# Kernel tuning notes

Measured on AMD Instinct MI355X. Metric: run time of the kernel, lower is better.

The kernel has to match this reference:

```python
import jax, jax.numpy as jnp
import numpy as np

B, V, J, H, W = 32, 2, 17, 128, 128
TEMP = 0.05   # SoftArgmax2D softmax_temp
EPS = 1e-12


def _soft_argmax(hm):
    # hm: (B*V, J, H, W) -> homogeneous coords (B*V, 3, J), per-joint max value
    bv, j, h, w = hm.shape
    p = jax.nn.softmax(hm.reshape(bv, j, h * w) / TEMP, axis=-1).reshape(bv, j, h, w)
    xs = jnp.arange(w, dtype=hm.dtype)
    ys = jnp.arange(h, dtype=hm.dtype)
    x = jnp.einsum('bjhw,w->bj', p, xs)
    y = jnp.einsum('bjhw,h->bj', p, ys)
    coords = jnp.stack([x, y, jnp.ones_like(x)], axis=1)  # (bv, 3, j)
    maxv = hm.max(axis=(-2, -1))
    return coords, maxv


def _skew(t):
    # t: (..., 3) -> skew-symmetric (..., 3, 3), matches -t_mat^T + t_mat in source
    tx, ty, tz = t[..., 0], t[..., 1], t[..., 2]
    z = jnp.zeros_like(tx)
    return jnp.stack([jnp.stack([z, -tz, ty], -1),
                      jnp.stack([tz, z, -tx], -1),
                      jnp.stack([-ty, tx, z], -1)], -2)


def _forward(origin_hms, AP_K, AP_T, LAT_K, LAT_T):
    K = jnp.stack([AP_K, LAT_K], axis=1)              # (B,V,3,3)
    T = jnp.stack([AP_T, LAT_T], axis=1)              # (B,V,4,4)
    R = T[:, :, :3, :3]
    t_std = T[:, :, :3, 3]                            # (B,V,3) standard_cam_T

    # fundamental matrices for all ordered pairs: cam1 = view j, cam2 = view i
    r = jnp.einsum('bimk,bjnk->bijmn', R, R)          # R_i @ R_j^T
    t = t_std[:, :, None, :] - jnp.einsum('bijmn,bjn->bijm', r, t_std)
    M = jnp.einsum('bijmn,bijnk->bijmk', _skew(t), r)
    invK = jnp.linalg.inv(K)
    # F = invK_i^T @ [t]x @ r @ invK_j
    F = jnp.einsum('bipm,bijpq,bjql->bijml', invK, M, invK)  # (B,V,V,3,3)

    coords, maxv = _soft_argmax(origin_hms)           # (B*V,3,J), (B*V,J)
    inv_aff = jnp.diag(jnp.asarray([4.0, 4.0, 1.0], dtype=origin_hms.dtype))  # inverse of 0.25 scale
    img = jnp.einsum('mn,bvnj->bvmj', inv_aff, coords.reshape(B, V, 3, J))
    confi = maxv.reshape(B, V, J)

    # epipolar distances, fully vectorized over (b, i, j) pairs
    l = jnp.einsum('bijmn,bjnk->bijmk', F, img)       # epipolar lines in view i from joints of view j
    cv = img[:, :, None]                              # (B,V,1,3,J)
    num = jnp.sum(cv * l, axis=3) ** 2                # (B,V,V,J)
    lp = jnp.einsum('bijnm,bink->bijmk', F, img)      # F^T @ cv_joints
    div = l[..., 0, :] ** 2 + l[..., 1, :] ** 2 + lp[..., 0, :] ** 2 + lp[..., 1, :] ** 2
    dist_full = jnp.sqrt(num / (div + EPS))           # (B,V,V,J)

    others = np.asarray([[j for j in range(V) if j != i] for i in range(V)])  # (V,V-1)
    ii = np.repeat(np.arange(V)[:, None], V - 1, axis=1)
    distances = dist_full[:, ii, others]              # (B,V,V-1,J)

    # stand-in for ViewWeightNet: confidence minus mean epipolar error, softmax over views
    score = confi - distances.mean(axis=2)            # (B,V,J)
    vw = jax.nn.softmax(score, axis=1)                # (B,V,J)

    mv = jnp.where(maxv > 0.01, maxv, 1e6).reshape(B * V, J, 1, 1)
    hms_norm = origin_hms / mv
    hm4 = hms_norm.reshape(B, V, J, H, W)

    # cat order: self heatmap first, then other views (matches get_warp_weight / cat_hm layout)
    order = np.asarray([[i] + [j for j in range(V) if j != i] for i in range(V)])  # (V,V)
    cat_hm = hm4[:, order]                            # (B,V,V,J,H,W); identity-warp stand-in for CamFusionModule
    ww = vw[:, order]                                 # (B,V,V,J) warp weights
    fused_hm = jnp.sum(ww[..., None, None] * cat_hm, axis=2).reshape(B * V, J, H, W)

    coords2, _ = _soft_argmax(fused_hm)
    img2 = jnp.einsum('mn,bvnj->bvmj', inv_aff, coords2.reshape(B, V, 3, J))
    return img2[:, :, :2, :], fused_hm


def setup_inputs() -> dict:
    key = jax.random.key(0)
    k1, k2, k3, k4, k5 = jax.random.split(key, 5)
    hms = jax.random.uniform(k1, (B * V, J, H, W), dtype=jnp.float32)

    def make_K(k):
        f = 1000.0 + jax.random.normal(k, (B,)) * 10.0
        Km = jnp.zeros((B, 3, 3), dtype=jnp.float32)
        Km = Km.at[:, 0, 0].set(f).at[:, 1, 1].set(f)
        Km = Km.at[:, 0, 2].set(256.0).at[:, 1, 2].set(256.0).at[:, 2, 2].set(1.0)
        return Km

    def make_T(k):
        A = jax.random.normal(k, (B, 3, 3))
        Q, _ = jnp.linalg.qr(A)
        Q = Q * jnp.linalg.det(Q)[:, None, None]  # force det = +1 (proper rotation)
        t = jax.random.normal(jax.random.fold_in(k, 1), (B, 3, 1)) * 0.1 + jnp.asarray([0.0, 0.0, 5.0]).reshape(3, 1)
        bottom = jnp.tile(jnp.asarray([[[0.0, 0.0, 0.0, 1.0]]]), (B, 1, 1))
        return jnp.concatenate([jnp.concatenate([Q, t], axis=2), bottom], axis=1).astype(jnp.float32)

    return {"origin_hms": hms, "AP_K": make_K(k2), "AP_T": make_T(k3),
            "LAT_K": make_K(k4), "LAT_T": make_T(k5)}


def reference(origin_hms, AP_K, AP_T, LAT_K, LAT_T):
    return _forward(origin_hms, AP_K, AP_T, LAT_K, LAT_T)
```

## Files before the change

### kernel.cpp

```cpp
#include <hip/hip_runtime.h>
#include <math.h>

#define NB 32
#define NV 2
#define NJ 17
#define NH 128
#define NW 128
#define MAPN (NH * NW)
#define MAPN4 (MAPN / 4)
#define NMAPS (NB * NV * NJ)
#define NBJ (NB * NJ)
#define OUT0N (NB * NV * 2 * NJ)
#define INV_TEMP 20.0f
#define EPS_D 1e-12f

typedef float vfloat4 __attribute__((ext_vector_type(4)));

__device__ __forceinline__ float waveMax(float v) {
#pragma unroll
    for (int off = 32; off > 0; off >>= 1)
        v = fmaxf(v, __shfl_xor(v, off, 64));
    return v;
}
__device__ __forceinline__ float waveSum(float v) {
#pragma unroll
    for (int off = 32; off > 0; off >>= 1)
        v += __shfl_xor(v, off, 64);
    return v;
}

__device__ __forceinline__ void inv3(const float K[3][3], float o[3][3]) {
    const float a = K[0][0], b = K[0][1], c = K[0][2];
    const float d = K[1][0], e = K[1][1], f = K[1][2];
    const float g = K[2][0], h = K[2][1], i = K[2][2];
    const float A =  (e * i - f * h);
    const float Bv = -(d * i - f * g);
    const float C =  (d * h - e * g);
    const float det = a * A + b * Bv + c * C;
    const float id = 1.0f / det;
    o[0][0] = A * id;  o[0][1] = -(b * i - c * h) * id;  o[0][2] = (b * f - c * e) * id;
    o[1][0] = Bv * id; o[1][1] = (a * i - c * g) * id;   o[1][2] = -(a * f - c * d) * id;
    o[2][0] = C * id;  o[2][1] = -(a * h - b * g) * id;  o[2][2] = (a * e - b * d) * id;
}

__global__ __launch_bounds__(512, 4) void k_all(const float* __restrict__ hms,
                                                const float* __restrict__ APK,
                                                const float* __restrict__ APT,
                                                const float* __restrict__ LATK,
                                                const float* __restrict__ LATT,
                                                float* __restrict__ out) {
    const int blk = blockIdx.x;
    const int b = blk / NJ, j = blk % NJ;
    const int tid = threadIdx.x;
    const int wid = tid >> 6, lane = tid & 63;

    const size_t m0 = ((size_t)(b * 2 + 0) * NJ + j) * MAPN4;
    const size_t m1 = ((size_t)(b * 2 + 1) * NJ + j) * MAPN4;
    const float4* A  = (const float4*)hms + m0;
    const float4* Bm = (const float4*)hms + m1;

    float4 va[8], vb[8];
#pragma unroll
    for (int u = 0; u < 8; ++u) {
        va[u] = A[tid + u * 512];
        vb[u] = Bm[tid + u * 512];
    }

    float mx0 = -1e30f, mx1 = -1e30f;
    float s0 = 0.f, sx0 = 0.f, sy0 = 0.f;
    float s1 = 0.f, sx1 = 0.f, sy1 = 0.f;
#pragma unroll
    for (int u = 0; u < 8; ++u) {
        const int e0 = (tid + u * 512) * 4;
        const float hh = (float)(e0 >> 7);
        const float ww = (float)(e0 & 127);
        {
            const float4 v = va[u];
            mx0 = fmaxf(mx0, fmaxf(fmaxf(v.x, v.y), fmaxf(v.z, v.w)));
            const float ea = __expf((v.x - 1.0f) * INV_TEMP);
            const float eb = __expf((v.y - 1.0f) * INV_TEMP);
            const float ec = __expf((v.z - 1.0f) * INV_TEMP);
            const float ed = __expf((v.w - 1.0f) * INV_TEMP);
            const float se = (ea + eb) + (ec + ed);
            s0 += se; sy0 += se * hh;
            sx0 += ea * ww + eb * (ww + 1.f) + ec * (ww + 2.f) + ed * (ww + 3.f);
        }
        {
            const float4 v = vb[u];
            mx1 = fmaxf(mx1, fmaxf(fmaxf(v.x, v.y), fmaxf(v.z, v.w)));
            const float ea = __expf((v.x - 1.0f) * INV_TEMP);
            const float eb = __expf((v.y - 1.0f) * INV_TEMP);
            const float ec = __expf((v.z - 1.0f) * INV_TEMP);
            const float ed = __expf((v.w - 1.0f) * INV_TEMP);
            const float se = (ea + eb) + (ec + ed);
            s1 += se; sy1 += se * hh;
            sx1 += ea * ww + eb * (ww + 1.f) + ec * (ww + 2.f) + ed * (ww + 3.f);
        }
    }

    __shared__ float red[8][8];
    __shared__ float wsh[2];
    mx0 = waveMax(mx0); mx1 = waveMax(mx1);
    s0 = waveSum(s0); sx0 = waveSum(sx0); sy0 = waveSum(sy0);
    s1 = waveSum(s1); sx1 = waveSum(sx1); sy1 = waveSum(sy1);
    if (lane == 0) {
        red[0][wid] = mx0; red[1][wid] = s0; red[2][wid] = sx0; red[3][wid] = sy0;
        red[4][wid] = mx1; red[5][wid] = s1; red[6][wid] = sx1; red[7][wid] = sy1;
    }
    __syncthreads();

    if (tid == 0) {
        float M0 = red[0][0], S0 = red[1][0], SX0 = red[2][0], SY0 = red[3][0];
        float M1 = red[4][0], S1 = red[5][0], SX1 = red[6][0], SY1 = red[7][0];
#pragma unroll
        for (int w = 1; w < 8; ++w) {
            M0 = fmaxf(M0, red[0][w]); S0 += red[1][w]; SX0 += red[2][w]; SY0 += red[3][w];
            M1 = fmaxf(M1, red[4][w]); S1 += red[5][w]; SX1 += red[6][w]; SY1 += red[7][w];
        }
        const float conf[2] = {M0, M1};
        float img[2][3];
        img[0][0] = 4.0f * (SX0 / S0); img[0][1] = 4.0f * (SY0 / S0); img[0][2] = 1.0f;
        img[1][0] = 4.0f * (SX1 / S1); img[1][1] = 4.0f * (SY1 / S1); img[1][2] = 1.0f;

        float Km[2][3][3], R[2][3][3], tr[2][3], iK[2][3][3];
        for (int r = 0; r < 3; ++r)
            for (int c = 0; c < 3; ++c) {
                Km[0][r][c] = APK[b * 9 + r * 3 + c];
                Km[1][r][c] = LATK[b * 9 + r * 3 + c];
                R[0][r][c] = APT[b * 16 + r * 4 + c];
                R[1][r][c] = LATT[b * 16 + r * 4 + c];
            }
        for (int r = 0; r < 3; ++r) {
            tr[0][r] = APT[b * 16 + r * 4 + 3];
            tr[1][r] = LATT[b * 16 + r * 4 + 3];
        }
        inv3(Km[0], iK[0]);
        inv3(Km[1], iK[1]);

        float F[2][3][3];
        for (int i = 0; i < 2; ++i) {
            const int jj = 1 - i;
            float r[3][3];
            for (int m = 0; m < 3; ++m)
                for (int n = 0; n < 3; ++n)
                    r[m][n] = R[i][m][0] * R[jj][n][0] + R[i][m][1] * R[jj][n][1] + R[i][m][2] * R[jj][n][2];
            float tv[3];
            for (int m = 0; m < 3; ++m)
                tv[m] = tr[i][m] - (r[m][0] * tr[jj][0] + r[m][1] * tr[jj][1] + r[m][2] * tr[jj][2]);
            const float S[3][3] = {{0.f, -tv[2], tv[1]}, {tv[2], 0.f, -tv[0]}, {-tv[1], tv[0], 0.f}};
            float M[3][3];
            for (int m = 0; m < 3; ++m)
                for (int n = 0; n < 3; ++n)
                    M[m][n] = S[m][0] * r[0][n] + S[m][1] * r[1][n] + S[m][2] * r[2][n];
            float tmp[3][3];
            for (int p = 0; p < 3; ++p)
                for (int l = 0; l < 3; ++l)
                    tmp[p][l] = M[p][0] * iK[jj][0][l] + M[p][1] * iK[jj][1][l] + M[p][2] * iK[jj][2][l];
            for (int m = 0; m < 3; ++m)
                for (int l = 0; l < 3; ++l)
                    F[i][m][l] = iK[i][0][m] * tmp[0][l] + iK[i][1][m] * tmp[1][l] + iK[i][2][m] * tmp[2][l];
        }

        float score[2];
        for (int i = 0; i < 2; ++i) {
            const int jj = 1 - i;
            const float l0 = F[i][0][0] * img[jj][0] + F[i][0][1] * img[jj][1] + F[i][0][2] * img[jj][2];
            const float l1 = F[i][1][0] * img[jj][0] + F[i][1][1] * img[jj][1] + F[i][1][2] * img[jj][2];
            const float l2 = F[i][2][0] * img[jj][0] + F[i][2][1] * img[jj][1] + F[i][2][2] * img[jj][2];
            const float sdot = img[i][0] * l0 + img[i][1] * l1 + img[i][2] * l2;
            const float num = sdot * sdot;
            const float lp0 = F[i][0][0] * img[i][0] + F[i][1][0] * img[i][1] + F[i][2][0] * img[i][2];
            const float lp1 = F[i][0][1] * img[i][0] + F[i][1][1] * img[i][1] + F[i][2][1] * img[i][2];
            const float dv = l0 * l0 + l1 * l1 + lp0 * lp0 + lp1 * lp1;
            score[i] = conf[i] - sqrtf(num / (dv + EPS_D));
        }

        const float mS = fmaxf(score[0], score[1]);
        const float e0 = __expf(score[0] - mS), e1 = __expf(score[1] - mS);
        const float inv = 1.0f / (e0 + e1);
        const float mv0 = conf[0] > 0.01f ? conf[0] : 1e6f;
        const float mv1 = conf[1] > 0.01f ? conf[1] : 1e6f;
        wsh[0] = (e0 * inv) / mv0;
        wsh[1] = (e1 * inv) / mv1;
    }
    __syncthreads();
    const float w0 = wsh[0];
    const float w1 = wsh[1];

    float* outhm = out + OUT0N;
    vfloat4* O0 = reinterpret_cast<vfloat4*>(outhm) + m0;
    vfloat4* O1 = reinterpret_cast<vfloat4*>(outhm) + m1;

    float s = 0.f, sx = 0.f, sy = 0.f;
#pragma unroll
    for (int u = 0; u < 8; ++u) {
        const int i4 = tid + u * 512;
        const float4 a = va[u];
        const float4 c = vb[u];
        vfloat4 f;
        f.x = w0 * a.x + w1 * c.x;
        f.y = w0 * a.y + w1 * c.y;
        f.z = w0 * a.z + w1 * c.z;
        f.w = w0 * a.w + w1 * c.w;
        __builtin_nontemporal_store(f, &O0[i4]);
        __builtin_nontemporal_store(f, &O1[i4]);
        const int e0 = i4 * 4;
        const float hh = (float)(e0 >> 7);
        const float ww = (float)(e0 & 127);
        const float ea = __expf((f.x - 1.0f) * INV_TEMP);
        const float eb = __expf((f.y - 1.0f) * INV_TEMP);
        const float ec = __expf((f.z - 1.0f) * INV_TEMP);
        const float ed = __expf((f.w - 1.0f) * INV_TEMP);
        const float se = (ea + eb) + (ec + ed);
        s += se; sy += se * hh;
        sx += ea * ww + eb * (ww + 1.f) + ec * (ww + 2.f) + ed * (ww + 3.f);
    }

    s = waveSum(s); sx = waveSum(sx); sy = waveSum(sy);
    if (lane == 0) { red[0][wid] = s; red[1][wid] = sx; red[2][wid] = sy; }
    __syncthreads();
    if (tid == 0) {
        float S = red[0][0], SX = red[1][0], SY = red[2][0];
#pragma unroll
        for (int w = 1; w < 8; ++w) { S += red[0][w]; SX += red[1][w]; SY += red[2][w]; }
        const float x4 = 4.0f * (SX / S);
        const float y4 = 4.0f * (SY / S);
        out[((b * 2 + 0) * 2 + 0) * NJ + j] = x4;
        out[((b * 2 + 0) * 2 + 1) * NJ + j] = y4;
        out[((b * 2 + 1) * 2 + 0) * NJ + j] = x4;
        out[((b * 2 + 1) * 2 + 1) * NJ + j] = y4;
    }
}

extern "C" void kernel_launch(void* const* d_in, const int* in_sizes, int n_in,
                              void* d_out, int out_size, void* d_ws, size_t ws_size,
                              hipStream_t stream) {
    const float* hms  = (const float*)d_in[0];
    const float* APK  = (const float*)d_in[1];
    const float* APT  = (const float*)d_in[2];
    const float* LATK = (const float*)d_in[3];
    const float* LATT = (const float*)d_in[4];
    float* out = (float*)d_out;

    k_all<<<NBJ, 512, 0, stream>>>(hms, APK, APT, LATK, LATT, out);
}
```

Measured before the change: 141.7 us.

## Compute F redundantly per thread, drop vb register cache, reload view-1 map

Every thread now computes the fundamental matrices and the fusion weights redundantly. This removes the single-thread serial section and one barrier round trip. The view-1 map is no longer kept in registers and is reloaded from global memory (likely an L2 hit) in the fuse pass, which cuts register pressure. The launch bound's minimum-blocks hint drops from 4 to 2 to give the compiler more register room. In exchange, each thread does more redundant scalar math and the kernel issues a second read of one input map.

```diff
diff --git a/kernel.cpp b/kernel.cpp
--- a/kernel.cpp
+++ b/kernel.cpp
@@ -43,7 +43,7 @@
     o[2][0] = C * id;  o[2][1] = -(a * h - b * g) * id;  o[2][2] = (a * e - b * d) * id;
 }
 
-__global__ __launch_bounds__(512, 4) void k_all(const float* __restrict__ hms,
+__global__ __launch_bounds__(512, 2) void k_one(const float* __restrict__ hms,
                                                 const float* __restrict__ APK,
                                                 const float* __restrict__ APT,
                                                 const float* __restrict__ LATK,
@@ -54,74 +54,8 @@
     const int tid = threadIdx.x;
     const int wid = tid >> 6, lane = tid & 63;
 
-    const size_t m0 = ((size_t)(b * 2 + 0) * NJ + j) * MAPN4;
-    const size_t m1 = ((size_t)(b * 2 + 1) * NJ + j) * MAPN4;
-    const float4* A  = (const float4*)hms + m0;
-    const float4* Bm = (const float4*)hms + m1;
-
-    float4 va[8], vb[8];
-#pragma unroll
-    for (int u = 0; u < 8; ++u) {
-        va[u] = A[tid + u * 512];
-        vb[u] = Bm[tid + u * 512];
-    }
-
-    float mx0 = -1e30f, mx1 = -1e30f;
-    float s0 = 0.f, sx0 = 0.f, sy0 = 0.f;
-    float s1 = 0.f, sx1 = 0.f, sy1 = 0.f;
-#pragma unroll
-    for (int u = 0; u < 8; ++u) {
-        const int e0 = (tid + u * 512) * 4;
-        const float hh = (float)(e0 >> 7);
-        const float ww = (float)(e0 & 127);
-        {
-            const float4 v = va[u];
-            mx0 = fmaxf(mx0, fmaxf(fmaxf(v.x, v.y), fmaxf(v.z, v.w)));
-            const float ea = __expf((v.x - 1.0f) * INV_TEMP);
-            const float eb = __expf((v.y - 1.0f) * INV_TEMP);
-            const float ec = __expf((v.z - 1.0f) * INV_TEMP);
-            const float ed = __expf((v.w - 1.0f) * INV_TEMP);
-            const float se = (ea + eb) + (ec + ed);
-            s0 += se; sy0 += se * hh;
-            sx0 += ea * ww + eb * (ww + 1.f) + ec * (ww + 2.f) + ed * (ww + 3.f);
-        }
-        {
-            const float4 v = vb[u];
-            mx1 = fmaxf(mx1, fmaxf(fmaxf(v.x, v.y), fmaxf(v.z, v.w)));
-            const float ea = __expf((v.x - 1.0f) * INV_TEMP);
-            const float eb = __expf((v.y - 1.0f) * INV_TEMP);
-            const float ec = __expf((v.z - 1.0f) * INV_TEMP);
-            const float ed = __expf((v.w - 1.0f) * INV_TEMP);
-            const float se = (ea + eb) + (ec + ed);
-            s1 += se; sy1 += se * hh;
-            sx1 += ea * ww + eb * (ww + 1.f) + ec * (ww + 2.f) + ed * (ww + 3.f);
-        }
-    }
-
-    __shared__ float red[8][8];
-    __shared__ float wsh[2];
-    mx0 = waveMax(mx0); mx1 = waveMax(mx1);
-    s0 = waveSum(s0); sx0 = waveSum(sx0); sy0 = waveSum(sy0);
-    s1 = waveSum(s1); sx1 = waveSum(sx1); sy1 = waveSum(sy1);
-    if (lane == 0) {
-        red[0][wid] = mx0; red[1][wid] = s0; red[2][wid] = sx0; red[3][wid] = sy0;
-        red[4][wid] = mx1; red[5][wid] = s1; red[6][wid] = sx1; red[7][wid] = sy1;
-    }
-    __syncthreads();
-
-    if (tid == 0) {
-        float M0 = red[0][0], S0 = red[1][0], SX0 = red[2][0], SY0 = red[3][0];
-        float M1 = red[4][0], S1 = red[5][0], SX1 = red[6][0], SY1 = red[7][0];
-#pragma unroll
-        for (int w = 1; w < 8; ++w) {
-            M0 = fmaxf(M0, red[0][w]); S0 += red[1][w]; SX0 += red[2][w]; SY0 += red[3][w];
-            M1 = fmaxf(M1, red[4][w]); S1 += red[5][w]; SX1 += red[6][w]; SY1 += red[7][w];
-        }
-        const float conf[2] = {M0, M1};
-        float img[2][3];
-        img[0][0] = 4.0f * (SX0 / S0); img[0][1] = 4.0f * (SY0 / S0); img[0][2] = 1.0f;
-        img[1][0] = 4.0f * (SX1 / S1); img[1][1] = 4.0f * (SY1 / S1); img[1][2] = 1.0f;
-
+    float F[2][3][3];
+    {
         float Km[2][3][3], R[2][3][3], tr[2][3], iK[2][3][3];
         for (int r = 0; r < 3; ++r)
             for (int c = 0; c < 3; ++c) {
@@ -137,7 +71,6 @@
         inv3(Km[0], iK[0]);
         inv3(Km[1], iK[1]);
 
-        float F[2][3][3];
         for (int i = 0; i < 2; ++i) {
             const int jj = 1 - i;
             float r[3][3];
@@ -160,6 +93,72 @@
                 for (int l = 0; l < 3; ++l)
                     F[i][m][l] = iK[i][0][m] * tmp[0][l] + iK[i][1][m] * tmp[1][l] + iK[i][2][m] * tmp[2][l];
         }
+    }
+
+    const int idx0 = (b * 2 + 0) * NJ + j;
+    const int idx1 = (b * 2 + 1) * NJ + j;
+    const size_t m0 = (size_t)idx0 * MAPN4;
+    const size_t m1 = (size_t)idx1 * MAPN4;
+    const float4* A  = (const float4*)hms + m0;
+    const float4* Bp = (const float4*)hms + m1;
+
+    float4 va[8];
+    float mx0 = -1e30f, s0 = 0.f, sx0 = 0.f, sy0 = 0.f;
+    float mx1 = -1e30f, s1 = 0.f, sx1 = 0.f, sy1 = 0.f;
+#pragma unroll
+    for (int u = 0; u < 8; ++u) {
+        const int i4 = tid + u * 512;
+        const float4 v = A[i4];
+        const float4 w = Bp[i4];
+        va[u] = v;
+        const int e0 = i4 * 4;
+        const float hh = (float)(e0 >> 7);
+        const float ww = (float)(e0 & 127);
+        {
+            mx0 = fmaxf(mx0, fmaxf(fmaxf(v.x, v.y), fmaxf(v.z, v.w)));
+            const float ea = __expf((v.x - 1.0f) * INV_TEMP);
+            const float eb = __expf((v.y - 1.0f) * INV_TEMP);
+            const float ec = __expf((v.z - 1.0f) * INV_TEMP);
+            const float ed = __expf((v.w - 1.0f) * INV_TEMP);
+            const float se = (ea + eb) + (ec + ed);
+            s0 += se; sy0 += se * hh;
+            sx0 += ea * ww + eb * (ww + 1.f) + ec * (ww + 2.f) + ed * (ww + 3.f);
+        }
+        {
+            mx1 = fmaxf(mx1, fmaxf(fmaxf(w.x, w.y), fmaxf(w.z, w.w)));
+            const float ea = __expf((w.x - 1.0f) * INV_TEMP);
+            const float eb = __expf((w.y - 1.0f) * INV_TEMP);
+            const float ec = __expf((w.z - 1.0f) * INV_TEMP);
+            const float ed = __expf((w.w - 1.0f) * INV_TEMP);
+            const float se = (ea + eb) + (ec + ed);
+            s1 += se; sy1 += se * hh;
+            sx1 += ea * ww + eb * (ww + 1.f) + ec * (ww + 2.f) + ed * (ww + 3.f);
+        }
+    }
+
+    __shared__ float red[8][8];
+    mx0 = waveMax(mx0); mx1 = waveMax(mx1);
+    s0 = waveSum(s0); sx0 = waveSum(sx0); sy0 = waveSum(sy0);
+    s1 = waveSum(s1); sx1 = waveSum(sx1); sy1 = waveSum(sy1);
+    if (lane == 0) {
+        red[0][wid] = mx0; red[1][wid] = s0; red[2][wid] = sx0; red[3][wid] = sy0;
+        red[4][wid] = mx1; red[5][wid] = s1; red[6][wid] = sx1; red[7][wid] = sy1;
+    }
+    __syncthreads();
+    float M0 = red[0][0], S0 = red[1][0], SX0 = red[2][0], SY0 = red[3][0];
+    float M1 = red[4][0], S1 = red[5][0], SX1 = red[6][0], SY1 = red[7][0];
+#pragma unroll
+    for (int w = 1; w < 8; ++w) {
+        M0 = fmaxf(M0, red[0][w]); S0 += red[1][w]; SX0 += red[2][w]; SY0 += red[3][w];
+        M1 = fmaxf(M1, red[4][w]); S1 += red[5][w]; SX1 += red[6][w]; SY1 += red[7][w];
+    }
+
+    float w0, w1;
+    {
+        const float conf[2] = {M0, M1};
+        float img[2][3];
+        img[0][0] = 4.0f * (SX0 / S0); img[0][1] = 4.0f * (SY0 / S0); img[0][2] = 1.0f;
+        img[1][0] = 4.0f * (SX1 / S1); img[1][1] = 4.0f * (SY1 / S1); img[1][2] = 1.0f;
 
         float score[2];
         for (int i = 0; i < 2; ++i) {
@@ -174,18 +173,14 @@
             const float dv = l0 * l0 + l1 * l1 + lp0 * lp0 + lp1 * lp1;
             score[i] = conf[i] - sqrtf(num / (dv + EPS_D));
         }
-
         const float mS = fmaxf(score[0], score[1]);
-        const float e0 = __expf(score[0] - mS), e1 = __expf(score[1] - mS);
-        const float inv = 1.0f / (e0 + e1);
+        const float e0w = __expf(score[0] - mS), e1w = __expf(score[1] - mS);
+        const float inv = 1.0f / (e0w + e1w);
         const float mv0 = conf[0] > 0.01f ? conf[0] : 1e6f;
         const float mv1 = conf[1] > 0.01f ? conf[1] : 1e6f;
-        wsh[0] = (e0 * inv) / mv0;
-        wsh[1] = (e1 * inv) / mv1;
-    }
-    __syncthreads();
-    const float w0 = wsh[0];
-    const float w1 = wsh[1];
+        w0 = (e0w * inv) / mv0;
+        w1 = (e1w * inv) / mv1;
+    }
 
     float* outhm = out + OUT0N;
     vfloat4* O0 = reinterpret_cast<vfloat4*>(outhm) + m0;
@@ -196,7 +191,7 @@
     for (int u = 0; u < 8; ++u) {
         const int i4 = tid + u * 512;
         const float4 a = va[u];
-        const float4 c = vb[u];
+        const float4 c = Bp[i4];
         vfloat4 f;
         f.x = w0 * a.x + w1 * c.x;
         f.y = w0 * a.y + w1 * c.y;
@@ -216,6 +211,7 @@
         sx += ea * ww + eb * (ww + 1.f) + ec * (ww + 2.f) + ed * (ww + 3.f);
     }
 
+    __syncthreads();
     s = waveSum(s); sx = waveSum(sx); sy = waveSum(sy);
     if (lane == 0) { red[0][wid] = s; red[1][wid] = sx; red[2][wid] = sy; }
     __syncthreads();
@@ -242,5 +238,5 @@
     const float* LATT = (const float*)d_in[4];
     float* out = (float*)d_out;
 
-    k_all<<<NBJ, 512, 0, stream>>>(hms, APK, APT, LATK, LATT, out);
-}
+    k_one<<<NBJ, 512, 0, stream>>>(hms, APK, APT, LATK, LATT, out);
+}
```

After: 137.3 us. -3.1%, faster.
